# Kernel optimization log

Measured on AMD Instinct MI355X. Metric: run time of the kernel, lower is better.

Reference implementation:

```python
import jax, jax.numpy as jnp
import numpy as np

BN_EPS = 1e-5


def _bn_relu(h, gamma, beta):
    # BatchNorm1d in training mode: normalize over (batch, length) per channel
    mean = h.mean(axis=(0, 2), keepdims=True)
    var = h.var(axis=(0, 2), keepdims=True)
    h = (h - mean) * jax.lax.rsqrt(var + BN_EPS)
    h = h * gamma[None, :, None] + beta[None, :, None]
    return jax.nn.relu(h)


def _gather(ldesc, idx):
    # ldesc: [B, D, N], idx: [B, M] -> [B, D, M]
    B, D, N = ldesc.shape
    M = idx.shape[1]
    return jnp.take_along_axis(ldesc, jnp.broadcast_to(idx[:, None, :], (B, D, M)), axis=2)


def _scatter_mean(src, idx, N):
    # per-batch scatter-mean: src [B, D, M], idx [B, M] -> [B, D, N]
    def one(s, i):
        D = s.shape[0]
        sums = jnp.zeros((D, N), s.dtype).at[:, i].add(s)
        cnts = jnp.zeros((N,), s.dtype).at[i].add(1.0)
        return sums / jnp.maximum(cnts, 1.0)[None, :]
    return jax.vmap(one)(src, idx)


def _endpoint_update(ldesc, line_enc, idx, W1, b1, g1, bt1, W2, b2):
    B, D, _ = ldesc.shape
    ld = _gather(ldesc, idx)                                   # [B, D, 2L]
    # flip endpoint pairs: neighbor endpoint of each endpoint
    neigh = ld.reshape(B, D, -1, 2)[..., ::-1].reshape(B, D, -1)
    msg = jnp.concatenate([ld, neigh, line_enc], axis=1)       # [B, 3D, 2L]
    h = jnp.einsum('oc,bcm->bom', W1, msg) + b1[None, :, None]  # Conv1d k=1
    h = _bn_relu(h, g1, bt1)
    out = jnp.einsum('oc,bcm->bom', W2, h) + b2[None, :, None]
    return out                                                  # [B, D, 2L]


def setup_inputs() -> dict:
    key = jax.random.key(0)
    ks = jax.random.split(key, 12)
    B, D, N, M = 8, 256, 8192, 8192
    inp = {
        'ldesc0': jax.random.normal(ks[0], (B, D, N), jnp.float32),
        'ldesc1': jax.random.normal(ks[1], (B, D, N), jnp.float32),
        'line_enc0': jax.random.normal(ks[2], (B, D, M), jnp.float32),
        'line_enc1': jax.random.normal(ks[3], (B, D, M), jnp.float32),
        'lines_junc_idx0': jax.random.randint(ks[4], (B, M), 0, N),
        'lines_junc_idx1': jax.random.randint(ks[5], (B, M), 0, N),
        'W1': jax.random.normal(ks[6], (2 * D, 3 * D), jnp.float32) * (1.0 / np.sqrt(3 * D)),
        'b1': jnp.zeros((2 * D,), jnp.float32),
        'g1': jnp.ones((2 * D,), jnp.float32),
        'bt1': jnp.zeros((2 * D,), jnp.float32),
        'W2': jax.random.normal(ks[7], (D, 2 * D), jnp.float32) * (1.0 / np.sqrt(2 * D)),
        'b2': jnp.zeros((D,), jnp.float32),
    }
    return inp


def reference(ldesc0, ldesc1, line_enc0, line_enc1, lines_junc_idx0, lines_junc_idx1,
              W1, b1, g1, bt1, W2, b2):
    N = ldesc0.shape[2]
    up0 = _endpoint_update(ldesc0, line_enc0, lines_junc_idx0, W1, b1, g1, bt1, W2, b2)
    up1 = _endpoint_update(ldesc1, line_enc1, lines_junc_idx1, W1, b1, g1, bt1, W2, b2)
    out0 = ldesc0 + _scatter_mean(up0, lines_junc_idx0, N)
    out1 = ldesc1 + _scatter_mean(up1, lines_junc_idx1, N)
    return (out0, out1)
```

## Files before the change

### kernel.cpp

```cpp
#include <hip/hip_runtime.h>
#include <hip/hip_bf16.h>

#define B_  8
#define D_  256
#define N_  8192
#define M_  8192
#define O1_ 512
#define K1_ 768
#define K2_ 512

typedef unsigned short u16;
typedef __attribute__((ext_vector_type(8))) short bf8;
typedef __attribute__((ext_vector_type(4))) float f4;

static __device__ __forceinline__ float bf2f(u16 u) {
    unsigned v = ((unsigned)u) << 16;
    return __uint_as_float(v);
}
static __device__ __forceinline__ u16 f2bf(float f) {
    __hip_bfloat16 h = __float2bfloat16(f);
    return *reinterpret_cast<u16*>(&h);
}
static __device__ __forceinline__ void gl_lds16(const u16* g, u16* l) {
    __builtin_amdgcn_global_load_lds((const __attribute__((address_space(1))) void*)g,
                                     (__attribute__((address_space(3))) void*)l, 16, 0, 0);
}

__global__ __launch_bounds__(256) void k_transpose_bf16(const float* __restrict__ src,
                                                        u16* __restrict__ dst, int R, int C) {
    __shared__ float t[32][33];
    const int b  = blockIdx.z;
    const int c0 = blockIdx.x * 32, r0 = blockIdx.y * 32;
    const int tx = threadIdx.x, ty = threadIdx.y;
    const float* s = src + (size_t)b * R * C;
    u16* d = dst + (size_t)b * C * R;
#pragma unroll
    for (int i = 0; i < 4; ++i) {
        int r = r0 + ty + i * 8;
        t[ty + i * 8][tx] = s[(size_t)r * C + (c0 + tx)];
    }
    __syncthreads();
#pragma unroll
    for (int i = 0; i < 4; ++i) {
        int c = c0 + ty + i * 8;
        d[(size_t)c * R + (r0 + tx)] = f2bf(t[tx][ty + i * 8]);
    }
}

__global__ __launch_bounds__(256) void k_convert_w(const float* __restrict__ W1, const float* __restrict__ W2,
                                                   u16* __restrict__ W1b, u16* __restrict__ W2b) {
    int i = blockIdx.x * 256 + threadIdx.x;
    const int n1 = O1_ * K1_;
    const int n2 = D_ * K2_;
    if (i < n1) W1b[i] = f2bf(W1[i]);
    int j = i - n1;
    if (j >= 0 && j < n2) W2b[j] = f2bf(W2[j]);
}

__global__ __launch_bounds__(256) void k_gemm1(const u16* __restrict__ W1b,
                                               const u16* __restrict__ Tld,
                                               const u16* __restrict__ Tle,
                                               const int* __restrict__ idx,
                                               const float* __restrict__ b1,
                                               u16* __restrict__ hbuf) {
    __shared__ u16 At[128 * 32];
    __shared__ u16 Bt[128 * 32];
    const int b  = blockIdx.z;
    const int o0 = blockIdx.y * 128;
    const int m0 = blockIdx.x * 128;
    const int tid = threadIdx.x;
    const int w = tid >> 6, l = tid & 63;
    const int lr = l >> 2;
    const int lc = (l & 3) * 8;

    const u16* pA[2]; const u16* pB0[2]; const u16* pB1[2]; const u16* pB2[2];
#pragma unroll
    for (int t = 0; t < 2; ++t) {
        int row = t * 64 + w * 16 + lr;
        pA[t] = W1b + (size_t)(o0 + row) * K1_ + lc;
        int m  = m0 + row;
        int na = idx[b * M_ + m];
        int nb = idx[b * M_ + (m ^ 1)];
        pB0[t] = Tld + (size_t)(b * N_ + na) * D_ + lc;
        pB1[t] = Tld + (size_t)(b * N_ + nb) * D_ + lc;
        pB2[t] = Tle + (size_t)(b * M_ + m) * D_ + lc;
    }

    const int wr = w >> 1, wc = w & 1;
    f4 acc[4][4];
#pragma unroll
    for (int i = 0; i < 4; ++i)
#pragma unroll
        for (int j = 0; j < 4; ++j) acc[i][j] = {0.f, 0.f, 0.f, 0.f};

    const int aoff = (wr * 64 + (l & 15)) * 32 + (l >> 4) * 8;
    const int boff = (wc * 64 + (l & 15)) * 32 + (l >> 4) * 8;

    for (int kk = 0; kk < 24; ++kk) {
        const int seg  = kk >> 3;
        const int coff = (kk & 7) * 32;
#pragma unroll
        for (int t = 0; t < 2; ++t) {
            gl_lds16(pA[t] + kk * 32, At + (t * 64 + w * 16) * 32);
            const u16* src = (seg == 0) ? (pB0[t] + coff)
                           : (seg == 1) ? (pB1[t] + coff)
                                        : (pB2[t] + coff);
            gl_lds16(src, Bt + (t * 64 + w * 16) * 32);
        }
        __syncthreads();
        bf8 aF[4], bF[4];
#pragma unroll
        for (int i = 0; i < 4; ++i) aF[i] = *reinterpret_cast<const bf8*>(&At[aoff + i * 16 * 32]);
#pragma unroll
        for (int j = 0; j < 4; ++j) bF[j] = *reinterpret_cast<const bf8*>(&Bt[boff + j * 16 * 32]);
#pragma unroll
        for (int i = 0; i < 4; ++i)
#pragma unroll
            for (int j = 0; j < 4; ++j)
                acc[i][j] = __builtin_amdgcn_mfma_f32_16x16x32_bf16(aF[i], bF[j], acc[i][j], 0, 0, 0);
        __syncthreads();
    }

#pragma unroll
    for (int j = 0; j < 4; ++j) {
        int m = m0 + wc * 64 + j * 16 + (l & 15);
        size_t rowbase = (size_t)(b * M_ + m) * O1_;
#pragma unroll
        for (int i = 0; i < 4; ++i) {
            int orow = o0 + wr * 64 + i * 16 + (l >> 4) * 4;
            ushort4 pk;
            pk.x = f2bf(acc[i][j].x + b1[orow + 0]);
            pk.y = f2bf(acc[i][j].y + b1[orow + 1]);
            pk.z = f2bf(acc[i][j].z + b1[orow + 2]);
            pk.w = f2bf(acc[i][j].w + b1[orow + 3]);
            *reinterpret_cast<ushort4*>(&hbuf[rowbase + orow]) = pk;
        }
    }
}

__global__ __launch_bounds__(256) void k_stats(const u16* __restrict__ hbuf, float* __restrict__ stats) {
    const int t = threadIdx.x;
    const size_t row0 = (size_t)blockIdx.x * 256;
    float s0 = 0.f, q0 = 0.f, s1 = 0.f, q1 = 0.f;
    for (int r = 0; r < 256; ++r) {
        const u16* p = hbuf + (row0 + r) * O1_;
        float v0 = bf2f(p[t]);
        float v1 = bf2f(p[t + 256]);
        s0 += v0; q0 += v0 * v0;
        s1 += v1; q1 += v1 * v1;
    }
    atomicAdd(&stats[t], s0);
    atomicAdd(&stats[O1_ + t], q0);
    atomicAdd(&stats[t + 256], s1);
    atomicAdd(&stats[O1_ + t + 256], q1);
}

__global__ void k_finalize_ac(const float* __restrict__ stats, const float* __restrict__ g1,
                              const float* __restrict__ bt1, float* __restrict__ ac) {
    int o = blockIdx.x * 256 + threadIdx.x;
    if (o >= O1_) return;
    const float inv = 1.0f / ((float)B_ * (float)M_);
    float mean = stats[o] * inv;
    float var  = stats[O1_ + o] * inv - mean * mean;
    var = fmaxf(var, 0.0f);
    float a = g1[o] * rsqrtf(var + 1e-5f);
    ac[o] = a;
    ac[O1_ + o] = bt1[o] - mean * a;
}

__global__ __launch_bounds__(256) void k_bnrelu(u16* __restrict__ hbuf, const float* __restrict__ ac) {
    const size_t nv = (size_t)B_ * M_ * (O1_ / 8);
    const size_t stride = (size_t)gridDim.x * blockDim.x;
    for (size_t i = (size_t)blockIdx.x * blockDim.x + threadIdx.x; i < nv; i += stride) {
        size_t e = i * 8;
        int o = (int)(e & (O1_ - 1));
        ushort4* p = reinterpret_cast<ushort4*>(&hbuf[e]);
        ushort4 v0 = p[0], v1 = p[1];
        ushort4 r0, r1;
        r0.x = f2bf(fmaxf(bf2f(v0.x) * ac[o + 0] + ac[O1_ + o + 0], 0.0f));
        r0.y = f2bf(fmaxf(bf2f(v0.y) * ac[o + 1] + ac[O1_ + o + 1], 0.0f));
        r0.z = f2bf(fmaxf(bf2f(v0.z) * ac[o + 2] + ac[O1_ + o + 2], 0.0f));
        r0.w = f2bf(fmaxf(bf2f(v0.w) * ac[o + 3] + ac[O1_ + o + 3], 0.0f));
        r1.x = f2bf(fmaxf(bf2f(v1.x) * ac[o + 4] + ac[O1_ + o + 4], 0.0f));
        r1.y = f2bf(fmaxf(bf2f(v1.y) * ac[o + 5] + ac[O1_ + o + 5], 0.0f));
        r1.z = f2bf(fmaxf(bf2f(v1.z) * ac[o + 6] + ac[O1_ + o + 6], 0.0f));
        r1.w = f2bf(fmaxf(bf2f(v1.w) * ac[o + 7] + ac[O1_ + o + 7], 0.0f));
        p[0] = r0; p[1] = r1;
    }
}

__global__ void k_count_int(const int* __restrict__ idx, int* __restrict__ cnt) {
    int i = blockIdx.x * 256 + threadIdx.x;
    if (i < B_ * M_) atomicAdd(&cnt[(i >> 13) * N_ + idx[i]], 1);
}

__global__ __launch_bounds__(1024) void k_scan(const int* __restrict__ cnt, int* __restrict__ offs,
                                               int* __restrict__ fill) {
    __shared__ int wsum[1024];
    const int b = blockIdx.x;
    const int t = threadIdx.x;
    const int base = b * N_;
    int v[8]; int s = 0;
#pragma unroll
    for (int k = 0; k < 8; ++k) { v[k] = cnt[base + t * 8 + k]; s += v[k]; }
    wsum[t] = s;
    __syncthreads();
    for (int off = 1; off < 1024; off <<= 1) {
        int add = (t >= off) ? wsum[t - off] : 0;
        __syncthreads();
        wsum[t] += add;
        __syncthreads();
    }
    int run = (t > 0) ? wsum[t - 1] : 0;
#pragma unroll
    for (int k = 0; k < 8; ++k) {
        offs[base + t * 8 + k] = run;
        fill[base + t * 8 + k] = run;
        run += v[k];
    }
}

__global__ void k_fill(const int* __restrict__ idx, int* __restrict__ fill, int* __restrict__ mlist) {
    int i = blockIdx.x * 256 + threadIdx.x;
    if (i < B_ * M_) {
        int b = i >> 13, m = i & (M_ - 1);
        int pos = atomicAdd(&fill[b * N_ + idx[i]], 1);
        mlist[(size_t)b * M_ + pos] = m;
    }
}

__global__ __launch_bounds__(256) void k_gemm2(const u16* __restrict__ W2b,
                                               const u16* __restrict__ hbuf,
                                               const float* __restrict__ b2,
                                               u16* __restrict__ up) {
    __shared__ u16 At[128 * 32];
    __shared__ u16 Bt[128 * 32];
    const int b  = blockIdx.z;
    const int d0 = blockIdx.y * 128;
    const int m0 = blockIdx.x * 128;
    const int tid = threadIdx.x;
    const int w = tid >> 6, l = tid & 63;
    const int lr = l >> 2, lc = (l & 3) * 8;

    const u16* pA[2]; const u16* pB[2];
#pragma unroll
    for (int t = 0; t < 2; ++t) {
        int row = t * 64 + w * 16 + lr;
        pA[t] = W2b + (size_t)(d0 + row) * K2_ + lc;
        int m  = m0 + row;
        pB[t] = hbuf + (size_t)(b * M_ + m) * O1_ + lc;
    }
    const int wr = w >> 1, wc = w & 1;
    f4 acc[4][4];
#pragma unroll
    for (int i = 0; i < 4; ++i)
#pragma unroll
        for (int j = 0; j < 4; ++j) acc[i][j] = {0.f, 0.f, 0.f, 0.f};

    const int aoff = (wr * 64 + (l & 15)) * 32 + (l >> 4) * 8;
    const int boff = (wc * 64 + (l & 15)) * 32 + (l >> 4) * 8;

    for (int kk = 0; kk < 16; ++kk) {
#pragma unroll
        for (int t = 0; t < 2; ++t) {
            gl_lds16(pA[t] + kk * 32, At + (t * 64 + w * 16) * 32);
            gl_lds16(pB[t] + kk * 32, Bt + (t * 64 + w * 16) * 32);
        }
        __syncthreads();
        bf8 aF[4], bF[4];
#pragma unroll
        for (int i = 0; i < 4; ++i) aF[i] = *reinterpret_cast<const bf8*>(&At[aoff + i * 16 * 32]);
#pragma unroll
        for (int j = 0; j < 4; ++j) bF[j] = *reinterpret_cast<const bf8*>(&Bt[boff + j * 16 * 32]);
#pragma unroll
        for (int i = 0; i < 4; ++i)
#pragma unroll
            for (int j = 0; j < 4; ++j)
                acc[i][j] = __builtin_amdgcn_mfma_f32_16x16x32_bf16(aF[i], bF[j], acc[i][j], 0, 0, 0);
        __syncthreads();
    }

#pragma unroll
    for (int j = 0; j < 4; ++j) {
        int m = m0 + wc * 64 + j * 16 + (l & 15);
        size_t rowbase = (size_t)(b * M_ + m) * D_;
#pragma unroll
        for (int i = 0; i < 4; ++i) {
            int d = d0 + wr * 64 + i * 16 + (l >> 4) * 4;
            ushort4 pk;
            pk.x = f2bf(acc[i][j].x + b2[d + 0]);
            pk.y = f2bf(acc[i][j].y + b2[d + 1]);
            pk.z = f2bf(acc[i][j].z + b2[d + 2]);
            pk.w = f2bf(acc[i][j].w + b2[d + 3]);
            *reinterpret_cast<ushort4*>(&up[rowbase + d]) = pk;
        }
    }
}

__global__ __launch_bounds__(256) void k_reduce_finalize(const float* __restrict__ ldesc,
                                                         const u16* __restrict__ up,
                                                         const int* __restrict__ cnt,
                                                         const int* __restrict__ offs,
                                                         const int* __restrict__ mlist,
                                                         float* __restrict__ out) {
    __shared__ float lds[32][257];
    const int b  = blockIdx.z;
    const int n0 = blockIdx.x * 32;
    const int tx = threadIdx.x, ty = threadIdx.y;
#pragma unroll
    for (int i = 0; i < 4; ++i) {
        int nl = ty + i * 8;
        int n  = n0 + nl;
        int c   = cnt[b * N_ + n];
        int off = offs[b * N_ + n];
        float inv = 1.0f / (float)max(c, 1);
        float acc[8] = {0.f, 0.f, 0.f, 0.f, 0.f, 0.f, 0.f, 0.f};
        for (int e = 0; e < c; ++e) {
            int m = mlist[(size_t)b * M_ + off + e];
            const ushort4* row = reinterpret_cast<const ushort4*>(up + (size_t)(b * M_ + m) * D_ + tx * 8);
            ushort4 aa = row[0], bb = row[1];
            acc[0] += bf2f(aa.x); acc[1] += bf2f(aa.y); acc[2] += bf2f(aa.z); acc[3] += bf2f(aa.w);
            acc[4] += bf2f(bb.x); acc[5] += bf2f(bb.y); acc[6] += bf2f(bb.z); acc[7] += bf2f(bb.w);
        }
#pragma unroll
        for (int k = 0; k < 8; ++k) lds[nl][tx * 8 + k] = acc[k] * inv;
    }
    __syncthreads();
#pragma unroll
    for (int i = 0; i < 32; ++i) {
        int d = ty + i * 8;
        size_t o2 = (size_t)(b * D_ + d) * N_ + n0 + tx;
        out[o2] = ldesc[o2] + lds[tx][d];
    }
}

__global__ void k_marker(float* out, float v) { out[0] = v; }

extern "C" void kernel_launch(void* const* d_in, const int* in_sizes, int n_in,
                              void* d_out, int out_size, void* d_ws, size_t ws_size,
                              hipStream_t stream) {
    const float* ldesc0 = (const float*)d_in[0];
    const float* ldesc1 = (const float*)d_in[1];
    const float* le0    = (const float*)d_in[2];
    const float* le1    = (const float*)d_in[3];
    const int*   idx0   = (const int*)d_in[4];
    const int*   idx1   = (const int*)d_in[5];
    const float* W1     = (const float*)d_in[6];
    const float* b1     = (const float*)d_in[7];
    const float* g1     = (const float*)d_in[8];
    const float* bt1    = (const float*)d_in[9];
    const float* W2     = (const float*)d_in[10];
    const float* b2     = (const float*)d_in[11];
    float* out = (float*)d_out;

    char* ws = (char*)d_ws;
    const size_t oTld   = 0;
    const size_t oTle   = 33554432;
    const size_t oH     = 67108864;
    const size_t oW1b   = 134217728;
    const size_t oW2b   = oW1b + 786432;
    const size_t oStats = oW2b + 262144;
    const size_t oAC    = oStats + 4096;
    const size_t NEED   = oAC + 4096;
    if (ws_size < NEED) {
        k_marker<<<1, 1, 0, stream>>>(out, 1000.0f + (float)(ws_size >> 20));
        return;
    }
    u16*   Tld   = (u16*)(ws + oTld);
    u16*   up    = (u16*)(ws + oTld);
    u16*   Tle   = (u16*)(ws + oTle);
    int*   cnt   = (int*)(ws + oTle);
    int*   offs  = (int*)(ws + oTle + 262144);
    int*   fill  = (int*)(ws + oTle + 524288);
    int*   mlist = (int*)(ws + oTle + 786432);
    u16*   hbuf  = (u16*)(ws + oH);
    u16*   W1b   = (u16*)(ws + oW1b);
    u16*   W2b   = (u16*)(ws + oW2b);
    float* stats = (float*)(ws + oStats);
    float* ac    = (float*)(ws + oAC);

    k_convert_w<<<2048, 256, 0, stream>>>(W1, W2, W1b, W2b);

    const dim3 tb(32, 8);
    for (int s = 0; s < 2; ++s) {
        const float* ld  = s ? ldesc1 : ldesc0;
        const float* le  = s ? le1 : le0;
        const int*   idx = s ? idx1 : idx0;
        float* outp = out + (size_t)s * B_ * D_ * N_;

        k_transpose_bf16<<<dim3(N_ / 32, D_ / 32, B_), tb, 0, stream>>>(ld, Tld, D_, N_);
        k_transpose_bf16<<<dim3(M_ / 32, D_ / 32, B_), tb, 0, stream>>>(le, Tle, D_, M_);
        k_gemm1<<<dim3(M_ / 128, O1_ / 128, B_), 256, 0, stream>>>(W1b, Tld, Tle, idx, b1, hbuf);
        hipMemsetAsync(stats, 0, 4096, stream);
        k_stats<<<256, 256, 0, stream>>>(hbuf, stats);
        k_finalize_ac<<<2, 256, 0, stream>>>(stats, g1, bt1, ac);
        k_bnrelu<<<2048, 256, 0, stream>>>(hbuf, ac);
        hipMemsetAsync(cnt, 0, (size_t)B_ * N_ * 4, stream);
        k_count_int<<<B_ * M_ / 256, 256, 0, stream>>>(idx, cnt);
        k_scan<<<B_, 1024, 0, stream>>>(cnt, offs, fill);
        k_fill<<<B_ * M_ / 256, 256, 0, stream>>>(idx, fill, mlist);
        k_gemm2<<<dim3(M_ / 128, D_ / 128, B_), 256, 0, stream>>>(W2b, hbuf, b2, up);
        k_reduce_finalize<<<dim3(N_ / 32, 1, B_), tb, 0, stream>>>(ld, up, cnt, offs, mlist, outp);
    }
}
```

Baseline: 505.5 us.

## Fuse BN statistics into GEMM1 epilogue and BN+ReLU into GEMM2 B-load

Batch-norm sum and sum-of-squares are now reduced in the GEMM1 epilogue, using shuffles, LDS and per-block atomics, instead of a separate pass over hbuf. The BN affine transform and ReLU are applied while GEMM2 loads its B tile, via registers and LDS stores, which removes the standalone bnrelu read-modify-write. This cuts several full passes over the B*M*512 bf16 hidden buffer. The cost is that GEMM2's async global-to-LDS B load becomes a synchronous register path, and the statistics are taken from fp32 accumulators rather than bf16-rounded values.

```diff
diff --git a/kernel.cpp b/kernel.cpp
--- a/kernel.cpp
+++ b/kernel.cpp
@@ -62,7 +62,8 @@
                                                const u16* __restrict__ Tle,
                                                const int* __restrict__ idx,
                                                const float* __restrict__ b1,
-                                               u16* __restrict__ hbuf) {
+                                               u16* __restrict__ hbuf,
+                                               float* __restrict__ stats) {
     __shared__ u16 At[128 * 32];
     __shared__ u16 Bt[128 * 32];
     const int b  = blockIdx.z;
@@ -122,6 +123,43 @@
     }
 
 #pragma unroll
+    for (int i = 0; i < 4; ++i) {
+        int orow = o0 + wr * 64 + i * 16 + (l >> 4) * 4;
+        float b0v = b1[orow + 0], b1v = b1[orow + 1], b2v = b1[orow + 2], b3v = b1[orow + 3];
+#pragma unroll
+        for (int j = 0; j < 4; ++j) {
+            acc[i][j].x += b0v; acc[i][j].y += b1v; acc[i][j].z += b2v; acc[i][j].w += b3v;
+        }
+    }
+
+    float* redS = (float*)At;
+    float* redQ = (float*)At + 256;
+#pragma unroll
+    for (int i = 0; i < 4; ++i) {
+#pragma unroll
+        for (int r = 0; r < 4; ++r) {
+            float s = acc[i][0][r] + acc[i][1][r] + acc[i][2][r] + acc[i][3][r];
+            float q = acc[i][0][r] * acc[i][0][r] + acc[i][1][r] * acc[i][1][r]
+                    + acc[i][2][r] * acc[i][2][r] + acc[i][3][r] * acc[i][3][r];
+#pragma unroll
+            for (int mm = 1; mm < 16; mm <<= 1) {
+                s += __shfl_xor(s, mm, 16);
+                q += __shfl_xor(q, mm, 16);
+            }
+            if ((l & 15) == 0) {
+                int ch = wr * 64 + i * 16 + (l >> 4) * 4 + r;
+                redS[ch * 2 + wc] = s;
+                redQ[ch * 2 + wc] = q;
+            }
+        }
+    }
+    __syncthreads();
+    if (tid < 128) {
+        atomicAdd(&stats[o0 + tid],        redS[tid * 2] + redS[tid * 2 + 1]);
+        atomicAdd(&stats[O1_ + o0 + tid],  redQ[tid * 2] + redQ[tid * 2 + 1]);
+    }
+
+#pragma unroll
     for (int j = 0; j < 4; ++j) {
         int m = m0 + wc * 64 + j * 16 + (l & 15);
         size_t rowbase = (size_t)(b * M_ + m) * O1_;
@@ -129,30 +167,13 @@
         for (int i = 0; i < 4; ++i) {
             int orow = o0 + wr * 64 + i * 16 + (l >> 4) * 4;
             ushort4 pk;
-            pk.x = f2bf(acc[i][j].x + b1[orow + 0]);
-            pk.y = f2bf(acc[i][j].y + b1[orow + 1]);
-            pk.z = f2bf(acc[i][j].z + b1[orow + 2]);
-            pk.w = f2bf(acc[i][j].w + b1[orow + 3]);
+            pk.x = f2bf(acc[i][j].x);
+            pk.y = f2bf(acc[i][j].y);
+            pk.z = f2bf(acc[i][j].z);
+            pk.w = f2bf(acc[i][j].w);
             *reinterpret_cast<ushort4*>(&hbuf[rowbase + orow]) = pk;
         }
     }
-}
-
-__global__ __launch_bounds__(256) void k_stats(const u16* __restrict__ hbuf, float* __restrict__ stats) {
-    const int t = threadIdx.x;
-    const size_t row0 = (size_t)blockIdx.x * 256;
-    float s0 = 0.f, q0 = 0.f, s1 = 0.f, q1 = 0.f;
-    for (int r = 0; r < 256; ++r) {
-        const u16* p = hbuf + (row0 + r) * O1_;
-        float v0 = bf2f(p[t]);
-        float v1 = bf2f(p[t + 256]);
-        s0 += v0; q0 += v0 * v0;
-        s1 += v1; q1 += v1 * v1;
-    }
-    atomicAdd(&stats[t], s0);
-    atomicAdd(&stats[O1_ + t], q0);
-    atomicAdd(&stats[t + 256], s1);
-    atomicAdd(&stats[O1_ + t + 256], q1);
 }
 
 __global__ void k_finalize_ac(const float* __restrict__ stats, const float* __restrict__ g1,
@@ -168,27 +189,6 @@
     ac[O1_ + o] = bt1[o] - mean * a;
 }
 
-__global__ __launch_bounds__(256) void k_bnrelu(u16* __restrict__ hbuf, const float* __restrict__ ac) {
-    const size_t nv = (size_t)B_ * M_ * (O1_ / 8);
-    const size_t stride = (size_t)gridDim.x * blockDim.x;
-    for (size_t i = (size_t)blockIdx.x * blockDim.x + threadIdx.x; i < nv; i += stride) {
-        size_t e = i * 8;
-        int o = (int)(e & (O1_ - 1));
-        ushort4* p = reinterpret_cast<ushort4*>(&hbuf[e]);
-        ushort4 v0 = p[0], v1 = p[1];
-        ushort4 r0, r1;
-        r0.x = f2bf(fmaxf(bf2f(v0.x) * ac[o + 0] + ac[O1_ + o + 0], 0.0f));
-        r0.y = f2bf(fmaxf(bf2f(v0.y) * ac[o + 1] + ac[O1_ + o + 1], 0.0f));
-        r0.z = f2bf(fmaxf(bf2f(v0.z) * ac[o + 2] + ac[O1_ + o + 2], 0.0f));
-        r0.w = f2bf(fmaxf(bf2f(v0.w) * ac[o + 3] + ac[O1_ + o + 3], 0.0f));
-        r1.x = f2bf(fmaxf(bf2f(v1.x) * ac[o + 4] + ac[O1_ + o + 4], 0.0f));
-        r1.y = f2bf(fmaxf(bf2f(v1.y) * ac[o + 5] + ac[O1_ + o + 5], 0.0f));
-        r1.z = f2bf(fmaxf(bf2f(v1.z) * ac[o + 6] + ac[O1_ + o + 6], 0.0f));
-        r1.w = f2bf(fmaxf(bf2f(v1.w) * ac[o + 7] + ac[O1_ + o + 7], 0.0f));
-        p[0] = r0; p[1] = r1;
-    }
-}
-
 __global__ void k_count_int(const int* __restrict__ idx, int* __restrict__ cnt) {
     int i = blockIdx.x * 256 + threadIdx.x;
     if (i < B_ * M_) atomicAdd(&cnt[(i >> 13) * N_ + idx[i]], 1);
@@ -231,10 +231,12 @@
 
 __global__ __launch_bounds__(256) void k_gemm2(const u16* __restrict__ W2b,
                                                const u16* __restrict__ hbuf,
+                                               const float* __restrict__ ac,
                                                const float* __restrict__ b2,
                                                u16* __restrict__ up) {
     __shared__ u16 At[128 * 32];
     __shared__ u16 Bt[128 * 32];
+    __shared__ float acs[1024];
     const int b  = blockIdx.z;
     const int d0 = blockIdx.y * 128;
     const int m0 = blockIdx.x * 128;
@@ -242,6 +244,11 @@
     const int w = tid >> 6, l = tid & 63;
     const int lr = l >> 2, lc = (l & 3) * 8;
 
+    acs[tid]       = ac[tid];
+    acs[tid + 256] = ac[tid + 256];
+    acs[tid + 512] = ac[tid + 512];
+    acs[tid + 768] = ac[tid + 768];
+
     const u16* pA[2]; const u16* pB[2];
 #pragma unroll
     for (int t = 0; t < 2; ++t) {
@@ -259,12 +266,31 @@
 
     const int aoff = (wr * 64 + (l & 15)) * 32 + (l >> 4) * 8;
     const int boff = (wc * 64 + (l & 15)) * 32 + (l >> 4) * 8;
+    const int bdst = (w * 16 + lr) * 32 + lc;
+
+    __syncthreads();
 
     for (int kk = 0; kk < 16; ++kk) {
+        const int o = kk * 32 + lc;
+        f4 A0 = *reinterpret_cast<const f4*>(&acs[o]);
+        f4 A1 = *reinterpret_cast<const f4*>(&acs[o + 4]);
+        f4 C0 = *reinterpret_cast<const f4*>(&acs[512 + o]);
+        f4 C1 = *reinterpret_cast<const f4*>(&acs[512 + o + 4]);
 #pragma unroll
         for (int t = 0; t < 2; ++t) {
             gl_lds16(pA[t] + kk * 32, At + (t * 64 + w * 16) * 32);
-            gl_lds16(pB[t] + kk * 32, Bt + (t * 64 + w * 16) * 32);
+            const ushort4* ps = reinterpret_cast<const ushort4*>(pB[t] + kk * 32);
+            ushort4 v0 = ps[0], v1 = ps[1];
+            union { ushort4 u4[2]; bf8 v8; } pk;
+            pk.u4[0].x = f2bf(fmaxf(bf2f(v0.x) * A0.x + C0.x, 0.0f));
+            pk.u4[0].y = f2bf(fmaxf(bf2f(v0.y) * A0.y + C0.y, 0.0f));
+            pk.u4[0].z = f2bf(fmaxf(bf2f(v0.z) * A0.z + C0.z, 0.0f));
+            pk.u4[0].w = f2bf(fmaxf(bf2f(v0.w) * A0.w + C0.w, 0.0f));
+            pk.u4[1].x = f2bf(fmaxf(bf2f(v1.x) * A1.x + C1.x, 0.0f));
+            pk.u4[1].y = f2bf(fmaxf(bf2f(v1.y) * A1.y + C1.y, 0.0f));
+            pk.u4[1].z = f2bf(fmaxf(bf2f(v1.z) * A1.z + C1.z, 0.0f));
+            pk.u4[1].w = f2bf(fmaxf(bf2f(v1.w) * A1.w + C1.w, 0.0f));
+            *reinterpret_cast<bf8*>(&Bt[t * 64 * 32 + bdst]) = pk.v8;
         }
         __syncthreads();
         bf8 aF[4], bF[4];
@@ -390,16 +416,14 @@
 
         k_transpose_bf16<<<dim3(N_ / 32, D_ / 32, B_), tb, 0, stream>>>(ld, Tld, D_, N_);
         k_transpose_bf16<<<dim3(M_ / 32, D_ / 32, B_), tb, 0, stream>>>(le, Tle, D_, M_);
-        k_gemm1<<<dim3(M_ / 128, O1_ / 128, B_), 256, 0, stream>>>(W1b, Tld, Tle, idx, b1, hbuf);
         hipMemsetAsync(stats, 0, 4096, stream);
-        k_stats<<<256, 256, 0, stream>>>(hbuf, stats);
+        k_gemm1<<<dim3(M_ / 128, O1_ / 128, B_), 256, 0, stream>>>(W1b, Tld, Tle, idx, b1, hbuf, stats);
         k_finalize_ac<<<2, 256, 0, stream>>>(stats, g1, bt1, ac);
-        k_bnrelu<<<2048, 256, 0, stream>>>(hbuf, ac);
         hipMemsetAsync(cnt, 0, (size_t)B_ * N_ * 4, stream);
         k_count_int<<<B_ * M_ / 256, 256, 0, stream>>>(idx, cnt);
         k_scan<<<B_, 1024, 0, stream>>>(cnt, offs, fill);
         k_fill<<<B_ * M_ / 256, 256, 0, stream>>>(idx, fill, mlist);
-        k_gemm2<<<dim3(M_ / 128, D_ / 128, B_), 256, 0, stream>>>(W2b, hbuf, b2, up);
+        k_gemm2<<<dim3(M_ / 128, D_ / 128, B_), 256, 0, stream>>>(W2b, hbuf, ac, b2, up);
         k_reduce_finalize<<<dim3(N_ / 32, 1, B_), tb, 0, stream>>>(ld, up, cnt, offs, mlist, outp);
     }
 }
```

Result: faster. 488.8 us (-3.3%).
